# Kernel optimization log

Hardware: AMD Instinct MI355X
Metric: run time of the kernel (lower is better)

The kernel has to match this reference:

```python
import jax, jax.numpy as jnp
import numpy as np

N = 100000          # nodes
E = 3200000         # edges (avg degree 32)
C = 64              # classes
NUM_CORR = 10
ALPHA_CORR = 0.979
NUM_SMOOTH = 10
ALPHA_SMOOTH = 0.756


def setup_inputs() -> dict:
    key = jax.random.key(0)
    k1, k2, k3, k4, k5 = jax.random.split(key, 5)
    # soft predictions: rows sum to 1 (asserted in the torch code)
    y_soft = jax.nn.softmax(jax.random.normal(k1, (N, C), dtype=jnp.float32), axis=-1)
    labels = jax.random.randint(k2, (N,), 0, C)
    y_true = jax.nn.one_hot(labels, C, dtype=jnp.float32)
    src = jax.random.randint(k3, (E,), 0, N)
    dst = jax.random.randint(k4, (E,), 0, N)
    mask = jax.random.uniform(k5, (N,)) < 0.5
    return {"y_soft": y_soft, "y_true": y_true, "src": src, "dst": dst, "mask": mask}


def _propagate(y, src, dst, norm, num_layers, alpha, lo, hi):
    # DAD: y <- clip(last + alpha * D^-1/2 A D^-1/2 y, lo, hi) repeated
    last = (1.0 - alpha) * y
    for _ in range(num_layers):
        y = norm * y                                            # D^-1/2 y
        h = jax.ops.segment_sum(y[src], dst, num_segments=N)    # A (SpMM via copy_u/sum)
        y = alpha * h * norm                                    # alpha D^-1/2 (.)
        y = jnp.clip(last + y, lo, hi)                          # post_step clamp
    return y


def reference(y_soft, y_true, src, dst, mask):
    dt = y_soft.dtype
    degs = jnp.clip(jax.ops.segment_sum(jnp.ones((E,), dt), dst, num_segments=N), 1.0, None)
    norm = (degs ** -0.5)[:, None]                              # [N,1]
    m = mask[:, None]

    # ---- correct (autoscale=True) ----
    error = jnp.where(m, y_true - y_soft, jnp.zeros((), dt))    # zero off-mask
    smoothed_error = _propagate(error, src, dst, norm, NUM_CORR, ALPHA_CORR, -1.0, 1.0)
    numel = jnp.sum(mask).astype(dt)
    sigma = jnp.sum(jnp.abs(error)) / numel                     # error is 0 off-mask
    scale = sigma / jnp.sum(jnp.abs(smoothed_error), axis=1, keepdims=True)
    scale = jnp.where(jnp.isinf(scale) | (scale > 1000.0), jnp.ones((), dt), scale)
    result = y_soft + scale * smoothed_error
    result = jnp.where(jnp.isnan(result), y_soft, result)

    # ---- smooth ----
    y = jnp.where(m, y_true, result)                            # y_soft[mask] = y_true
    out = _propagate(y, src, dst, norm, NUM_SMOOTH, ALPHA_SMOOTH, 0.0, 1.0)
    return out
```

## Files before the change

kernel.cpp:

```cpp
#include <hip/hip_runtime.h>
#include <hip/hip_bf16.h>

#define NN 100000
#define EE 3200000
#define CC 64
#define NC (NN*CC)
#define SCAN_BLOCKS 391
#define ERR_BLOCKS 6250

__device__ __forceinline__ float ldf(const void* p, long i, int isbf) {
    if (isbf) {
        unsigned int u = ((const unsigned short*)p)[i];
        return __uint_as_float(u << 16);
    }
    return ((const float*)p)[i];
}

__device__ __forceinline__ float wave_sum(float a) {
    for (int m = 1; m < 64; m <<= 1) a += __shfl_xor(a, m, 64);
    return a;
}

__device__ __forceinline__ unsigned pack_bf16(float a, float b) {
    unsigned ua = __float_as_uint(a); ua = (ua + 0x7FFFu + ((ua >> 16) & 1u)) >> 16;
    unsigned ub = __float_as_uint(b); ub = (ub + 0x7FFFu + ((ub >> 16) & 1u)) >> 16;
    return ua | (ub << 16);
}

__global__ void detect_kernel(const void* ytrue, const void* mask, int* flags) {
    int t = threadIdx.x;
    const unsigned int* w = (const unsigned int*)ytrue;
    int nb = 0, nm = 0;
    for (int i = t; i < 16384; i += 256)
        if ((w[i] & 0xFFFFu) == 0x3F80u) nb = 1;
    const unsigned char* mb = (const unsigned char*)mask;
    for (int i = t; i < 4096; i += 256)
        if ((i & 3) != 0 && mb[i] != 0) nm = 1;
    if (nb) atomicOr(&flags[0], 1);
    if (nm) atomicOr(&flags[1], 1);
}

__global__ void prep_kernel(const void* ytrue, const void* mask, const int* flags,
                            int* __restrict__ label, float* __restrict__ mask01) {
    int gt = blockIdx.x * blockDim.x + threadIdx.x;
    int node = gt >> 6, lane = gt & 63;
    if (node >= NN) return;
    int isbf = flags[0];
    float tv = ldf(ytrue, (long)node * CC + lane, isbf);
    unsigned long long b = __ballot(tv > 0.5f);
    if (lane == 0) {
        label[node] = (b == 0ull) ? 0 : (__ffsll((long long)b) - 1);
        int mv = flags[1] ? (int)((const unsigned char*)mask)[node] : ((const int*)mask)[node];
        mask01[node] = mv ? 1.f : 0.f;
    }
}

__global__ void deg_kernel(const int* __restrict__ dst, int* __restrict__ degi) {
    int e = blockIdx.x * blockDim.x + threadIdx.x;
    if (e < EE) atomicAdd(&degi[dst[e]], 1);
}

__global__ void norm_kernel(const int* __restrict__ degi, float* __restrict__ norm) {
    int n = blockIdx.x * blockDim.x + threadIdx.x;
    if (n < NN) {
        int d = degi[n]; if (d < 1) d = 1;
        norm[n] = rsqrtf((float)d);
    }
}

__global__ void scan1_kernel(const int* __restrict__ degi, int* __restrict__ partials) {
    int t = threadIdx.x, i = blockIdx.x * 256 + t;
    __shared__ int sm[256];
    sm[t] = (i < NN) ? degi[i] : 0; __syncthreads();
    for (int s = 128; s > 0; s >>= 1) {
        if (t < s) sm[t] += sm[t + s];
        __syncthreads();
    }
    if (t == 0) partials[blockIdx.x] = sm[0];
}

__global__ void scan2_kernel(const int* __restrict__ partials, int* __restrict__ chunk_off) {
    int t = threadIdx.x;
    __shared__ int sm[512];
    int v = (t < SCAN_BLOCKS) ? partials[t] : 0;
    sm[t] = v; __syncthreads();
    for (int off = 1; off < 512; off <<= 1) {
        int x = (t >= off) ? sm[t - off] : 0;
        __syncthreads();
        sm[t] += x;
        __syncthreads();
    }
    chunk_off[t] = sm[t] - v;
}

__global__ void scan3_kernel(const int* __restrict__ degi, const int* __restrict__ chunk_off,
                             int* __restrict__ row_ptr, int* __restrict__ cursor) {
    int t = threadIdx.x, b = blockIdx.x, i = b * 256 + t;
    __shared__ int sm[256];
    int v = (i < NN) ? degi[i] : 0;
    sm[t] = v; __syncthreads();
    for (int off = 1; off < 256; off <<= 1) {
        int x = (t >= off) ? sm[t - off] : 0;
        __syncthreads();
        sm[t] += x;
        __syncthreads();
    }
    int base = chunk_off[b];
    if (i < NN) {
        int ex = base + sm[t] - v;
        row_ptr[i] = ex; cursor[i] = ex;
    }
    if (i == NN - 1) row_ptr[NN] = base + sm[t];
}

__global__ void fill_kernel(const int* __restrict__ src, const int* __restrict__ dst,
                            int* __restrict__ cursor, int* __restrict__ csr_src) {
    int e = blockIdx.x * blockDim.x + threadIdx.x;
    if (e < EE) {
        int pos = atomicAdd(&cursor[dst[e]], 1);
        csr_src[pos] = src[e];
    }
}

__global__ void err_kernel(const void* ysoft, const int* flags, const int* __restrict__ label,
                           const float* __restrict__ mask01, const float* __restrict__ norm,
                           float* __restrict__ base, unsigned* __restrict__ curn,
                           float* __restrict__ err_part) {
    int i4 = blockIdx.x * 256 + threadIdx.x;
    int node = i4 >> 4;
    int isbf = flags[0];
    float m = mask01[node];
    int lab = label[node];
    float nrm = norm[node];
    int c0 = (i4 & 15) * 4;
    float4 e;
    if (isbf) {
        ushort4 u = ((const ushort4*)ysoft)[i4];
        e.x = __uint_as_float((unsigned)u.x << 16);
        e.y = __uint_as_float((unsigned)u.y << 16);
        e.z = __uint_as_float((unsigned)u.z << 16);
        e.w = __uint_as_float((unsigned)u.w << 16);
    } else {
        e = ((const float4*)ysoft)[i4];
    }
    e.x = (m != 0.f) ? ((c0 + 0 == lab) ? 1.f : 0.f) - e.x : 0.f;
    e.y = (m != 0.f) ? ((c0 + 1 == lab) ? 1.f : 0.f) - e.y : 0.f;
    e.z = (m != 0.f) ? ((c0 + 2 == lab) ? 1.f : 0.f) - e.z : 0.f;
    e.w = (m != 0.f) ? ((c0 + 3 == lab) ? 1.f : 0.f) - e.w : 0.f;
    ((float4*)base)[i4] = e;
    ((uint2*)curn)[i4] = make_uint2(pack_bf16(e.x * nrm, e.y * nrm),
                                    pack_bf16(e.z * nrm, e.w * nrm));
    float a = fabsf(e.x) + fabsf(e.y) + fabsf(e.z) + fabsf(e.w);
    a = wave_sum(a);
    __shared__ float sm[4];
    if ((threadIdx.x & 63) == 0) sm[threadIdx.x >> 6] = a;
    __syncthreads();
    if (threadIdx.x == 0) err_part[blockIdx.x] = sm[0] + sm[1] + sm[2] + sm[3];
}

__global__ void reduce_kernel(const float* __restrict__ mask01,
                              const float* __restrict__ err_part, float* __restrict__ scal) {
    int t = threadIdx.x;
    float s0 = 0.f, s1 = 0.f;
    for (int i = t; i < NN; i += 1024) s0 += mask01[i];
    for (int i = t; i < ERR_BLOCKS; i += 1024) s1 += err_part[i];
    __shared__ float a0[1024], a1[1024];
    a0[t] = s0; a1[t] = s1; __syncthreads();
    for (int s = 512; s > 0; s >>= 1) {
        if (t < s) { a0[t] += a0[t + s]; a1[t] += a1[t + s]; }
        __syncthreads();
    }
    if (t == 0) { scal[0] = a0[0]; scal[1] = a1[0]; }
}

__global__ void gather_kernel(const int* __restrict__ row_ptr, const int* __restrict__ csr_src,
                              const unsigned* __restrict__ curn, const float* __restrict__ base,
                              const float* __restrict__ norm, void* __restrict__ out,
                              float* __restrict__ rowsum, const int* flags,
                              float alpha, float lo, float hi, int mode) {
    int gt = blockIdx.x * blockDim.x + threadIdx.x;
    int node = gt >> 6, lane = gt & 63;
    if (node >= NN) return;
    int hl = lane & 31;
    int half = lane >> 5;
    int beg = row_ptr[node], end = row_ptr[node + 1];
    float acc0 = 0.f, acc1 = 0.f, acc2 = 0.f, acc3 = 0.f;
    for (int eb = beg; eb < end; eb += 64) {
        int ne = end - eb; if (ne > 64) ne = 64;
        int sv = (eb + lane < end) ? csr_src[eb + lane] : 0;
        int j = 0;
        for (; j + 7 < ne; j += 8) {
            int sA = __shfl(sv, j + 0 + half, 64);
            int sB = __shfl(sv, j + 2 + half, 64);
            int sC = __shfl(sv, j + 4 + half, 64);
            int sD = __shfl(sv, j + 6 + half, 64);
            unsigned wA = curn[(long)sA * 32 + hl];
            unsigned wB = curn[(long)sB * 32 + hl];
            unsigned wC = curn[(long)sC * 32 + hl];
            unsigned wD = curn[(long)sD * 32 + hl];
            acc0 += __uint_as_float(wA << 16) + __uint_as_float(wC << 16);
            acc1 += __uint_as_float(wA & 0xFFFF0000u) + __uint_as_float(wC & 0xFFFF0000u);
            acc2 += __uint_as_float(wB << 16) + __uint_as_float(wD << 16);
            acc3 += __uint_as_float(wB & 0xFFFF0000u) + __uint_as_float(wD & 0xFFFF0000u);
        }
        for (; j < ne; j += 2) {
            int jj = j + half;
            float wt = (jj < ne) ? 1.f : 0.f;
            int s = __shfl(sv, (jj < ne) ? jj : j, 64);
            unsigned w = curn[(long)s * 32 + hl];
            acc0 += wt * __uint_as_float(w << 16);
            acc1 += wt * __uint_as_float(w & 0xFFFF0000u);
        }
    }
    acc0 += acc2; acc1 += acc3;
    acc0 += __shfl_xor(acc0, 32, 64);
    acc1 += __shfl_xor(acc1, 32, 64);

    float nrm = norm[node];
    long i2 = (long)node * 32 + hl;
    float2 b2 = ((const float2*)base)[i2];
    float v0 = (1.f - alpha) * b2.x + alpha * nrm * acc0;
    float v1 = (1.f - alpha) * b2.y + alpha * nrm * acc1;
    v0 = v0 < lo ? lo : (v0 > hi ? hi : v0);
    v1 = v1 < lo ? lo : (v1 > hi ? hi : v1);

    if (mode == 1) {
        float contrib = (lane < 32) ? (fabsf(v0) + fabsf(v1)) : 0.f;
        float rs = wave_sum(contrib);
        if (lane == 0) rowsum[node] = rs;
        if (lane < 32) ((float2*)out)[i2] = make_float2(v0, v1);
    } else if (mode == 0) {
        if (lane < 32) ((unsigned*)out)[i2] = pack_bf16(v0 * nrm, v1 * nrm);
    } else {
        if (lane < 32) {
            if (flags[0]) ((unsigned*)out)[i2] = pack_bf16(v0, v1);
            else          ((float2*)out)[i2] = make_float2(v0, v1);
        }
    }
}

__global__ void scale_kernel(const float* __restrict__ rowsum, const float* __restrict__ scal,
                             float* __restrict__ scale) {
    int n = blockIdx.x * blockDim.x + threadIdx.x;
    if (n >= NN) return;
    float sigma = scal[1] / scal[0];
    float s = sigma / rowsum[n];
    if (isinf(s) || s > 1000.f) s = 1.f;
    scale[n] = s;
}

__global__ void y0_kernel(const void* ysoft, const int* flags, const int* __restrict__ label,
                          const float* __restrict__ mask01, const float* __restrict__ scale,
                          const float* __restrict__ norm, const float* __restrict__ smoothed,
                          float* __restrict__ base, unsigned* __restrict__ curn) {
    int i4 = blockIdx.x * 256 + threadIdx.x;
    int node = i4 >> 4;
    int isbf = flags[0];
    float m = mask01[node];
    int lab = label[node];
    float nrm = norm[node], sc = scale[node];
    int c0 = (i4 & 15) * 4;
    float4 ys;
    if (isbf) {
        ushort4 u = ((const ushort4*)ysoft)[i4];
        ys.x = __uint_as_float((unsigned)u.x << 16);
        ys.y = __uint_as_float((unsigned)u.y << 16);
        ys.z = __uint_as_float((unsigned)u.z << 16);
        ys.w = __uint_as_float((unsigned)u.w << 16);
    } else {
        ys = ((const float4*)ysoft)[i4];
    }
    float4 sm = ((const float4*)smoothed)[i4];
    float rx = ys.x + sc * sm.x; if (isnan(rx)) rx = ys.x;
    float ry = ys.y + sc * sm.y; if (isnan(ry)) ry = ys.y;
    float rz = ys.z + sc * sm.z; if (isnan(rz)) rz = ys.z;
    float rw = ys.w + sc * sm.w; if (isnan(rw)) rw = ys.w;
    float4 y;
    y.x = (m != 0.f) ? ((c0 + 0 == lab) ? 1.f : 0.f) : rx;
    y.y = (m != 0.f) ? ((c0 + 1 == lab) ? 1.f : 0.f) : ry;
    y.z = (m != 0.f) ? ((c0 + 2 == lab) ? 1.f : 0.f) : rz;
    y.w = (m != 0.f) ? ((c0 + 3 == lab) ? 1.f : 0.f) : rw;
    ((float4*)base)[i4] = y;
    ((uint2*)curn)[i4] = make_uint2(pack_bf16(y.x * nrm, y.y * nrm),
                                    pack_bf16(y.z * nrm, y.w * nrm));
}

extern "C" void kernel_launch(void* const* d_in, const int* in_sizes, int n_in,
                              void* d_out, int out_size, void* d_ws, size_t ws_size,
                              hipStream_t stream) {
    const void* ysoft = d_in[0];
    const void* ytrue = d_in[1];
    const int* src = (const int*)d_in[2];
    const int* dst = (const int*)d_in[3];
    const void* mask = d_in[4];

    char* ws = (char*)d_ws;
    int*   flags     = (int*)ws;
    float* scal      = (float*)(ws + 64);
    int*   partials  = (int*)(ws + 4096);
    int*   chunk_off = (int*)(ws + 8192);
    float* err_part  = (float*)(ws + 12288);
    int*   degi      = (int*)(ws + 40960);
    size_t ZERO_BYTES = 40960 + (size_t)NN * 4;

    size_t off = (ZERO_BYTES + 255) & ~(size_t)255;
    int*   label   = (int*)(ws + off);   off += (size_t)NN * 4;
    float* mask01  = (float*)(ws + off); off += (size_t)NN * 4;
    float* norm    = (float*)(ws + off); off += (size_t)NN * 4;
    float* scale   = (float*)(ws + off); off += (size_t)NN * 4;
    float* rowsum  = (float*)(ws + off); off += (size_t)NN * 4;
    int*   row_ptr = (int*)(ws + off);   off += (size_t)(NN + 1) * 4;
    int*   cursor  = (int*)(ws + off);   off += (size_t)NN * 4;
    off = (off + 255) & ~(size_t)255;
    int*   csr_src  = (int*)(ws + off);      off += (size_t)EE * 4;
    off = (off + 255) & ~(size_t)255;
    float*    base     = (float*)(ws + off);    off += (size_t)NC * 4;
    float*    smoothed = (float*)(ws + off);    off += (size_t)NC * 4;
    unsigned* bufA     = (unsigned*)(ws + off); off += (size_t)NC * 2;
    unsigned* bufB     = (unsigned*)(ws + off); off += (size_t)NC * 2;

    hipMemsetAsync(ws, 0, ZERO_BYTES, stream);

    detect_kernel<<<1, 256, 0, stream>>>(ytrue, mask, flags);
    prep_kernel<<<(NN * 64 + 255) / 256, 256, 0, stream>>>(ytrue, mask, flags, label, mask01);
    deg_kernel<<<(EE + 255) / 256, 256, 0, stream>>>(dst, degi);
    norm_kernel<<<(NN + 255) / 256, 256, 0, stream>>>(degi, norm);
    scan1_kernel<<<SCAN_BLOCKS, 256, 0, stream>>>(degi, partials);
    scan2_kernel<<<1, 512, 0, stream>>>(partials, chunk_off);
    scan3_kernel<<<SCAN_BLOCKS, 256, 0, stream>>>(degi, chunk_off, row_ptr, cursor);
    fill_kernel<<<(EE + 255) / 256, 256, 0, stream>>>(src, dst, cursor, csr_src);
    err_kernel<<<ERR_BLOCKS, 256, 0, stream>>>(ysoft, flags, label, mask01, norm, base, bufA, err_part);
    reduce_kernel<<<1, 1024, 0, stream>>>(mask01, err_part, scal);

    const int gather_blocks = (NN * 64 + 255) / 256;

    unsigned* cur = bufA; unsigned* nxt = bufB;
    for (int l = 0; l < 10; l++) {
        int mode = (l < 9) ? 0 : 1;
        void* o = (l < 9) ? (void*)nxt : (void*)smoothed;
        gather_kernel<<<gather_blocks, 256, 0, stream>>>(row_ptr, csr_src, cur, base, norm, o,
                                                         rowsum, flags, 0.979f, -1.f, 1.f, mode);
        unsigned* t = cur; cur = nxt; nxt = t;
    }

    scale_kernel<<<(NN + 255) / 256, 256, 0, stream>>>(rowsum, scal, scale);
    y0_kernel<<<ERR_BLOCKS, 256, 0, stream>>>(ysoft, flags, label, mask01, scale, norm,
                                              smoothed, base, bufA);

    cur = bufA; nxt = bufB;
    for (int l = 0; l < 10; l++) {
        int mode = (l < 9) ? 0 : 3;
        void* o = (l < 9) ? (void*)nxt : (void*)d_out;
        gather_kernel<<<gather_blocks, 256, 0, stream>>>(row_ptr, csr_src, cur, base, norm, o,
                                                         rowsum, flags, 0.756f, 0.f, 1.f, mode);
        unsigned* t = cur; cur = nxt; nxt = t;
    }
}
```

Baseline: 1.790 ms.

## Split feature columns into four chunk-major slabs and gather per chunk

Re-lays out the propagated feature buffers as four 16-column chunks stored chunk-major. Each gather block then processes one chunk for four nodes, with 8 lanes per neighbor and 8 neighbors per step. The aim is a smaller per-iteration working set, about 3.2 MB of bf16 per chunk, so the random neighbor gathers hit cache better. In exchange each edge list is read four times, row sums are accumulated with atomics into a zeroed buffer, and the final output is scattered back to row-major order. Non-temporal loads are used for the edge indices and the base values.

Result: slower. 3.920 ms (+119.0%).

```diff
diff --git a/kernel.cpp b/kernel.cpp
--- a/kernel.cpp
+++ b/kernel.cpp
@@ -7,6 +7,7 @@
 #define NC (NN*CC)
 #define SCAN_BLOCKS 391
 #define ERR_BLOCKS 6250
+
 
 __device__ __forceinline__ float ldf(const void* p, long i, int isbf) {
     if (isbf) {
@@ -128,11 +129,14 @@
                            float* __restrict__ err_part) {
     int i4 = blockIdx.x * 256 + threadIdx.x;
     int node = i4 >> 4;
+    int w16 = i4 & 15;
+    int chunk = w16 >> 2, q = w16 & 3;
+    long ci = ((long)chunk * NN + node) * 4 + q;
     int isbf = flags[0];
     float m = mask01[node];
     int lab = label[node];
     float nrm = norm[node];
-    int c0 = (i4 & 15) * 4;
+    int c0 = w16 * 4;
     float4 e;
     if (isbf) {
         ushort4 u = ((const ushort4*)ysoft)[i4];
@@ -147,8 +151,8 @@
     e.y = (m != 0.f) ? ((c0 + 1 == lab) ? 1.f : 0.f) - e.y : 0.f;
     e.z = (m != 0.f) ? ((c0 + 2 == lab) ? 1.f : 0.f) - e.z : 0.f;
     e.w = (m != 0.f) ? ((c0 + 3 == lab) ? 1.f : 0.f) - e.w : 0.f;
-    ((float4*)base)[i4] = e;
-    ((uint2*)curn)[i4] = make_uint2(pack_bf16(e.x * nrm, e.y * nrm),
+    ((float4*)base)[ci] = e;
+    ((uint2*)curn)[ci] = make_uint2(pack_bf16(e.x * nrm, e.y * nrm),
                                     pack_bf16(e.z * nrm, e.w * nrm));
     float a = fabsf(e.x) + fabsf(e.y) + fabsf(e.z) + fabsf(e.w);
     a = wave_sum(a);
@@ -173,68 +177,76 @@
     if (t == 0) { scal[0] = a0[0]; scal[1] = a1[0]; }
 }
 
-__global__ void gather_kernel(const int* __restrict__ row_ptr, const int* __restrict__ csr_src,
-                              const unsigned* __restrict__ curn, const float* __restrict__ base,
-                              const float* __restrict__ norm, void* __restrict__ out,
-                              float* __restrict__ rowsum, const int* flags,
-                              float alpha, float lo, float hi, int mode) {
-    int gt = blockIdx.x * blockDim.x + threadIdx.x;
-    int node = gt >> 6, lane = gt & 63;
-    if (node >= NN) return;
-    int hl = lane & 31;
-    int half = lane >> 5;
+__global__ void __launch_bounds__(256)
+gather_kernel(const int* __restrict__ row_ptr, const int* __restrict__ csr_src,
+              const unsigned* __restrict__ curn, const float* __restrict__ base,
+              const float* __restrict__ norm, void* __restrict__ out,
+              float* __restrict__ rowsum, const int* flags,
+              float alpha, float lo, float hi, int mode) {
+    int chunk = blockIdx.x & 3;
+    int node = (blockIdx.x >> 2) * 4 + (threadIdx.x >> 6);
+    int lane = threadIdx.x & 63;
+    int group = lane >> 3, gl = lane & 7;
+    long cbase = (long)chunk * NN;
+    const unsigned* __restrict__ cw = curn + cbase * 8;
     int beg = row_ptr[node], end = row_ptr[node + 1];
-    float acc0 = 0.f, acc1 = 0.f, acc2 = 0.f, acc3 = 0.f;
+    float acc0 = 0.f, acc1 = 0.f;
     for (int eb = beg; eb < end; eb += 64) {
         int ne = end - eb; if (ne > 64) ne = 64;
-        int sv = (eb + lane < end) ? csr_src[eb + lane] : 0;
+        int sv = (eb + lane < end) ? __builtin_nontemporal_load(csr_src + eb + lane) : 0;
         int j = 0;
-        for (; j + 7 < ne; j += 8) {
-            int sA = __shfl(sv, j + 0 + half, 64);
-            int sB = __shfl(sv, j + 2 + half, 64);
-            int sC = __shfl(sv, j + 4 + half, 64);
-            int sD = __shfl(sv, j + 6 + half, 64);
-            unsigned wA = curn[(long)sA * 32 + hl];
-            unsigned wB = curn[(long)sB * 32 + hl];
-            unsigned wC = curn[(long)sC * 32 + hl];
-            unsigned wD = curn[(long)sD * 32 + hl];
-            acc0 += __uint_as_float(wA << 16) + __uint_as_float(wC << 16);
-            acc1 += __uint_as_float(wA & 0xFFFF0000u) + __uint_as_float(wC & 0xFFFF0000u);
-            acc2 += __uint_as_float(wB << 16) + __uint_as_float(wD << 16);
-            acc3 += __uint_as_float(wB & 0xFFFF0000u) + __uint_as_float(wD & 0xFFFF0000u);
+        for (; j + 31 < ne; j += 32) {
+            int s0 = __shfl(sv, j + group, 64);
+            int s1 = __shfl(sv, j + 8 + group, 64);
+            int s2 = __shfl(sv, j + 16 + group, 64);
+            int s3 = __shfl(sv, j + 24 + group, 64);
+            unsigned w0 = cw[(long)s0 * 8 + gl];
+            unsigned w1 = cw[(long)s1 * 8 + gl];
+            unsigned w2 = cw[(long)s2 * 8 + gl];
+            unsigned w3 = cw[(long)s3 * 8 + gl];
+            acc0 += __uint_as_float(w0 << 16) + __uint_as_float(w1 << 16)
+                  + __uint_as_float(w2 << 16) + __uint_as_float(w3 << 16);
+            acc1 += __uint_as_float(w0 & 0xFFFF0000u) + __uint_as_float(w1 & 0xFFFF0000u)
+                  + __uint_as_float(w2 & 0xFFFF0000u) + __uint_as_float(w3 & 0xFFFF0000u);
         }
-        for (; j < ne; j += 2) {
-            int jj = j + half;
-            float wt = (jj < ne) ? 1.f : 0.f;
-            int s = __shfl(sv, (jj < ne) ? jj : j, 64);
-            unsigned w = curn[(long)s * 32 + hl];
+        for (; j < ne; j += 8) {
+            int ej = j + group;
+            int s = __shfl(sv, (ej < ne) ? ej : j, 64);
+            float wt = (ej < ne) ? 1.f : 0.f;
+            unsigned w = cw[(long)s * 8 + gl];
             acc0 += wt * __uint_as_float(w << 16);
             acc1 += wt * __uint_as_float(w & 0xFFFF0000u);
         }
     }
-    acc0 += acc2; acc1 += acc3;
-    acc0 += __shfl_xor(acc0, 32, 64);
-    acc1 += __shfl_xor(acc1, 32, 64);
+    acc0 += __shfl_xor(acc0, 8, 64);  acc1 += __shfl_xor(acc1, 8, 64);
+    acc0 += __shfl_xor(acc0, 16, 64); acc1 += __shfl_xor(acc1, 16, 64);
+    acc0 += __shfl_xor(acc0, 32, 64); acc1 += __shfl_xor(acc1, 32, 64);
 
     float nrm = norm[node];
-    long i2 = (long)node * 32 + hl;
-    float2 b2 = ((const float2*)base)[i2];
+    long i2 = (cbase + node) * 8 + gl;
+    float2 b2;
+    {
+        const float* bp = base + i2 * 2;
+        b2.x = __builtin_nontemporal_load(bp);
+        b2.y = __builtin_nontemporal_load(bp + 1);
+    }
     float v0 = (1.f - alpha) * b2.x + alpha * nrm * acc0;
     float v1 = (1.f - alpha) * b2.y + alpha * nrm * acc1;
     v0 = v0 < lo ? lo : (v0 > hi ? hi : v0);
     v1 = v1 < lo ? lo : (v1 > hi ? hi : v1);
 
-    if (mode == 1) {
-        float contrib = (lane < 32) ? (fabsf(v0) + fabsf(v1)) : 0.f;
-        float rs = wave_sum(contrib);
-        if (lane == 0) rowsum[node] = rs;
-        if (lane < 32) ((float2*)out)[i2] = make_float2(v0, v1);
-    } else if (mode == 0) {
-        if (lane < 32) ((unsigned*)out)[i2] = pack_bf16(v0 * nrm, v1 * nrm);
+    if (mode == 0) {
+        if (lane < 8) ((unsigned*)out)[i2] = pack_bf16(v0 * nrm, v1 * nrm);
+    } else if (mode == 1) {
+        float rs = fabsf(v0) + fabsf(v1);
+        rs += __shfl_xor(rs, 1, 64); rs += __shfl_xor(rs, 2, 64); rs += __shfl_xor(rs, 4, 64);
+        if (lane == 0) atomicAdd(&rowsum[node], rs);
+        if (lane < 8) ((float2*)out)[i2] = make_float2(v0, v1);
     } else {
-        if (lane < 32) {
-            if (flags[0]) ((unsigned*)out)[i2] = pack_bf16(v0, v1);
-            else          ((float2*)out)[i2] = make_float2(v0, v1);
+        if (lane < 8) {
+            long oi = (long)node * 32 + chunk * 8 + gl;
+            if (flags[0]) ((unsigned*)out)[oi] = pack_bf16(v0, v1);
+            else          ((float2*)out)[oi] = make_float2(v0, v1);
         }
     }
 }
@@ -255,11 +267,14 @@
                           float* __restrict__ base, unsigned* __restrict__ curn) {
     int i4 = blockIdx.x * 256 + threadIdx.x;
     int node = i4 >> 4;
+    int w16 = i4 & 15;
+    int chunk = w16 >> 2, q = w16 & 3;
+    long ci = ((long)chunk * NN + node) * 4 + q;
     int isbf = flags[0];
     float m = mask01[node];
     int lab = label[node];
     float nrm = norm[node], sc = scale[node];
-    int c0 = (i4 & 15) * 4;
+    int c0 = w16 * 4;
     float4 ys;
     if (isbf) {
         ushort4 u = ((const ushort4*)ysoft)[i4];
@@ -270,7 +285,7 @@
     } else {
         ys = ((const float4*)ysoft)[i4];
     }
-    float4 sm = ((const float4*)smoothed)[i4];
+    float4 sm = ((const float4*)smoothed)[ci];
     float rx = ys.x + sc * sm.x; if (isnan(rx)) rx = ys.x;
     float ry = ys.y + sc * sm.y; if (isnan(ry)) ry = ys.y;
     float rz = ys.z + sc * sm.z; if (isnan(rz)) rz = ys.z;
@@ -280,8 +295,8 @@
     y.y = (m != 0.f) ? ((c0 + 1 == lab) ? 1.f : 0.f) : ry;
     y.z = (m != 0.f) ? ((c0 + 2 == lab) ? 1.f : 0.f) : rz;
     y.w = (m != 0.f) ? ((c0 + 3 == lab) ? 1.f : 0.f) : rw;
-    ((float4*)base)[i4] = y;
-    ((uint2*)curn)[i4] = make_uint2(pack_bf16(y.x * nrm, y.y * nrm),
+    ((float4*)base)[ci] = y;
+    ((uint2*)curn)[ci] = make_uint2(pack_bf16(y.x * nrm, y.y * nrm),
                                     pack_bf16(y.z * nrm, y.w * nrm));
 }
 
@@ -301,14 +316,14 @@
     int*   chunk_off = (int*)(ws + 8192);
     float* err_part  = (float*)(ws + 12288);
     int*   degi      = (int*)(ws + 40960);
-    size_t ZERO_BYTES = 40960 + (size_t)NN * 4;
+    float* rowsum    = (float*)(ws + 40960 + (size_t)NN * 4);
+    size_t ZERO_BYTES = 40960 + (size_t)NN * 8;
 
     size_t off = (ZERO_BYTES + 255) & ~(size_t)255;
     int*   label   = (int*)(ws + off);   off += (size_t)NN * 4;
     float* mask01  = (float*)(ws + off); off += (size_t)NN * 4;
     float* norm    = (float*)(ws + off); off += (size_t)NN * 4;
     float* scale   = (float*)(ws + off); off += (size_t)NN * 4;
-    float* rowsum  = (float*)(ws + off); off += (size_t)NN * 4;
     int*   row_ptr = (int*)(ws + off);   off += (size_t)(NN + 1) * 4;
     int*   cursor  = (int*)(ws + off);   off += (size_t)NN * 4;
     off = (off + 255) & ~(size_t)255;
@@ -332,7 +347,7 @@
     err_kernel<<<ERR_BLOCKS, 256, 0, stream>>>(ysoft, flags, label, mask01, norm, base, bufA, err_part);
     reduce_kernel<<<1, 1024, 0, stream>>>(mask01, err_part, scal);
 
-    const int gather_blocks = (NN * 64 + 255) / 256;
+    const int gather_blocks = NN;
 
     unsigned* cur = bufA; unsigned* nxt = bufB;
     for (int l = 0; l < 10; l++) {
```

## Build CSR via two-level bucket sort instead of global atomic counting sort

Applied to the files above, without the earlier changes.

Replaces the global-atomic degree count, three-kernel scan and atomic scatter fill with a bucketed two-pass sort. Edges are first binned by dst>>8 using shared-memory histograms and staging into a temporary buffer that aliases `base`. Each bucket is then sorted locally in LDS to produce row_ptr, norm and csr_src. The aim is to cut contended global atomics and scattered writes during CSR construction. It also folds scale_kernel into y0_kernel. The cost is extra passes over the edge list, 64KB of LDS staging per block, and a dependence on `base` not being needed before err_kernel.

After: 1.498 ms. 1.2x faster.

```diff
diff --git a/kernel.cpp b/kernel.cpp
--- a/kernel.cpp
+++ b/kernel.cpp
@@ -5,8 +5,10 @@
 #define EE 3200000
 #define CC 64
 #define NC (NN*CC)
-#define SCAN_BLOCKS 391
 #define ERR_BLOCKS 6250
+#define NB 391
+#define TILE 8192
+#define NTILE 391
 
 __device__ __forceinline__ float ldf(const void* p, long i, int isbf) {
     if (isbf) {
@@ -55,34 +57,25 @@
     }
 }
 
-__global__ void deg_kernel(const int* __restrict__ dst, int* __restrict__ degi) {
-    int e = blockIdx.x * blockDim.x + threadIdx.x;
-    if (e < EE) atomicAdd(&degi[dst[e]], 1);
-}
-
-__global__ void norm_kernel(const int* __restrict__ degi, float* __restrict__ norm) {
-    int n = blockIdx.x * blockDim.x + threadIdx.x;
-    if (n < NN) {
-        int d = degi[n]; if (d < 1) d = 1;
-        norm[n] = rsqrtf((float)d);
-    }
-}
-
-__global__ void scan1_kernel(const int* __restrict__ degi, int* __restrict__ partials) {
-    int t = threadIdx.x, i = blockIdx.x * 256 + t;
-    __shared__ int sm[256];
-    sm[t] = (i < NN) ? degi[i] : 0; __syncthreads();
-    for (int s = 128; s > 0; s >>= 1) {
-        if (t < s) sm[t] += sm[t + s];
-        __syncthreads();
-    }
-    if (t == 0) partials[blockIdx.x] = sm[0];
-}
-
-__global__ void scan2_kernel(const int* __restrict__ partials, int* __restrict__ chunk_off) {
+__global__ void histA_kernel(const int* __restrict__ dst, int* __restrict__ bucket_tot) {
+    __shared__ int hist[NB];
+    int t = threadIdx.x;
+    for (int b = t; b < NB; b += 256) hist[b] = 0;
+    __syncthreads();
+    int e0 = blockIdx.x * TILE;
+    int n = EE - e0; if (n > TILE) n = TILE;
+    for (int k = t; k < n; k += 256)
+        atomicAdd(&hist[dst[e0 + k] >> 8], 1);
+    __syncthreads();
+    for (int b = t; b < NB; b += 256)
+        if (hist[b]) atomicAdd(&bucket_tot[b], hist[b]);
+}
+
+__global__ void bscan_kernel(const int* __restrict__ bucket_tot,
+                             int* __restrict__ bucket_base, int* __restrict__ bucket_fill) {
     int t = threadIdx.x;
     __shared__ int sm[512];
-    int v = (t < SCAN_BLOCKS) ? partials[t] : 0;
+    int v = (t < NB) ? bucket_tot[t] : 0;
     sm[t] = v; __syncthreads();
     for (int off = 1; off < 512; off <<= 1) {
         int x = (t >= off) ? sm[t - off] : 0;
@@ -90,14 +83,66 @@
         sm[t] += x;
         __syncthreads();
     }
-    chunk_off[t] = sm[t] - v;
-}
-
-__global__ void scan3_kernel(const int* __restrict__ degi, const int* __restrict__ chunk_off,
-                             int* __restrict__ row_ptr, int* __restrict__ cursor) {
-    int t = threadIdx.x, b = blockIdx.x, i = b * 256 + t;
-    __shared__ int sm[256];
-    int v = (i < NN) ? degi[i] : 0;
+    int ex = sm[t] - v;
+    if (t <= NB) { bucket_base[t] = ex; bucket_fill[t] = ex; }
+}
+
+__global__ void __launch_bounds__(512)
+binA_kernel(const int* __restrict__ src, const int* __restrict__ dst,
+            int* __restrict__ bucket_fill, uint2* __restrict__ tmp) {
+    __shared__ uint2 stage[TILE];
+    __shared__ int hist[512], hofs[512], curL[512], gbase[512];
+    __shared__ int sm[512];
+    int t = threadIdx.x;
+    int e0 = blockIdx.x * TILE;
+    int n = EE - e0; if (n > TILE) n = TILE;
+
+    hist[t] = 0;
+    __syncthreads();
+    for (int k = t; k < n; k += 512)
+        atomicAdd(&hist[dst[e0 + k] >> 8], 1);
+    __syncthreads();
+    int v = hist[t];
+    sm[t] = v; __syncthreads();
+    for (int off = 1; off < 512; off <<= 1) {
+        int x = (t >= off) ? sm[t - off] : 0;
+        __syncthreads();
+        sm[t] += x;
+        __syncthreads();
+    }
+    hofs[t] = sm[t] - v;
+    curL[t] = sm[t] - v;
+    __syncthreads();
+    for (int k = t; k < n; k += 512) {
+        int s = src[e0 + k], d = dst[e0 + k];
+        int b = d >> 8;
+        int p = atomicAdd(&curL[b], 1);
+        stage[p] = make_uint2((unsigned)s, (unsigned)d);
+    }
+    if (t < NB) {
+        int c = hist[t];
+        gbase[t] = c ? atomicAdd(&bucket_fill[t], c) : 0;
+    }
+    __syncthreads();
+    for (int k = t; k < n; k += 512) {
+        uint2 pr = stage[k];
+        int b = (int)(pr.y >> 8);
+        tmp[gbase[b] + (k - hofs[b])] = pr;
+    }
+}
+
+__global__ void __launch_bounds__(256)
+csrB_kernel(const uint2* __restrict__ tmp, const int* __restrict__ bucket_base,
+            int* __restrict__ row_ptr, float* __restrict__ norm, int* __restrict__ csr_src) {
+    __shared__ int deg[256], cur[256], sm[256];
+    int t = threadIdx.x, b = blockIdx.x;
+    int ebeg = bucket_base[b], eend = bucket_base[b + 1];
+    deg[t] = 0;
+    __syncthreads();
+    for (int i = ebeg + t; i < eend; i += 256)
+        atomicAdd(&deg[tmp[i].y & 255u], 1);
+    __syncthreads();
+    int v = deg[t];
     sm[t] = v; __syncthreads();
     for (int off = 1; off < 256; off <<= 1) {
         int x = (t >= off) ? sm[t - off] : 0;
@@ -105,20 +150,20 @@
         sm[t] += x;
         __syncthreads();
     }
-    int base = chunk_off[b];
-    if (i < NN) {
-        int ex = base + sm[t] - v;
-        row_ptr[i] = ex; cursor[i] = ex;
-    }
-    if (i == NN - 1) row_ptr[NN] = base + sm[t];
-}
-
-__global__ void fill_kernel(const int* __restrict__ src, const int* __restrict__ dst,
-                            int* __restrict__ cursor, int* __restrict__ csr_src) {
-    int e = blockIdx.x * blockDim.x + threadIdx.x;
-    if (e < EE) {
-        int pos = atomicAdd(&cursor[dst[e]], 1);
-        csr_src[pos] = src[e];
+    int lofs = sm[t] - v;
+    int node = b * 256 + t;
+    if (node < NN) {
+        row_ptr[node] = ebeg + lofs;
+        int d = v; if (d < 1) d = 1;
+        norm[node] = rsqrtf((float)d);
+    }
+    if (b == NB - 1 && t == 0) row_ptr[NN] = EE;
+    cur[t] = lofs;
+    __syncthreads();
+    for (int i = ebeg + t; i < eend; i += 256) {
+        uint2 pr = tmp[i];
+        int p = atomicAdd(&cur[pr.y & 255u], 1);
+        csr_src[ebeg + p] = (int)pr.x;
     }
 }
 
@@ -239,18 +284,9 @@
     }
 }
 
-__global__ void scale_kernel(const float* __restrict__ rowsum, const float* __restrict__ scal,
-                             float* __restrict__ scale) {
-    int n = blockIdx.x * blockDim.x + threadIdx.x;
-    if (n >= NN) return;
-    float sigma = scal[1] / scal[0];
-    float s = sigma / rowsum[n];
-    if (isinf(s) || s > 1000.f) s = 1.f;
-    scale[n] = s;
-}
-
 __global__ void y0_kernel(const void* ysoft, const int* flags, const int* __restrict__ label,
-                          const float* __restrict__ mask01, const float* __restrict__ scale,
+                          const float* __restrict__ mask01, const float* __restrict__ rowsum,
+                          const float* __restrict__ scal,
                           const float* __restrict__ norm, const float* __restrict__ smoothed,
                           float* __restrict__ base, unsigned* __restrict__ curn) {
     int i4 = blockIdx.x * 256 + threadIdx.x;
@@ -258,7 +294,10 @@
     int isbf = flags[0];
     float m = mask01[node];
     int lab = label[node];
-    float nrm = norm[node], sc = scale[node];
+    float nrm = norm[node];
+    float sigma = scal[1] / scal[0];
+    float sc = sigma / rowsum[node];
+    if (isinf(sc) || sc > 1000.f) sc = 1.f;
     int c0 = (i4 & 15) * 4;
     float4 ys;
     if (isbf) {
@@ -295,40 +334,38 @@
     const void* mask = d_in[4];
 
     char* ws = (char*)d_ws;
-    int*   flags     = (int*)ws;
-    float* scal      = (float*)(ws + 64);
-    int*   partials  = (int*)(ws + 4096);
-    int*   chunk_off = (int*)(ws + 8192);
-    float* err_part  = (float*)(ws + 12288);
-    int*   degi      = (int*)(ws + 40960);
-    size_t ZERO_BYTES = 40960 + (size_t)NN * 4;
-
-    size_t off = (ZERO_BYTES + 255) & ~(size_t)255;
+    int*   flags       = (int*)ws;
+    float* scal        = (float*)(ws + 64);
+    int*   bucket_tot  = (int*)(ws + 4096);
+    size_t ZERO_BYTES  = 16384;
+    int*   bucket_base = (int*)(ws + 16384);
+    int*   bucket_fill = (int*)(ws + 20480);
+    float* err_part    = (float*)(ws + 24576);
+
+    size_t off = 24576 + (size_t)ERR_BLOCKS * 4;
+    off = (off + 255) & ~(size_t)255;
     int*   label   = (int*)(ws + off);   off += (size_t)NN * 4;
     float* mask01  = (float*)(ws + off); off += (size_t)NN * 4;
     float* norm    = (float*)(ws + off); off += (size_t)NN * 4;
-    float* scale   = (float*)(ws + off); off += (size_t)NN * 4;
     float* rowsum  = (float*)(ws + off); off += (size_t)NN * 4;
     int*   row_ptr = (int*)(ws + off);   off += (size_t)(NN + 1) * 4;
-    int*   cursor  = (int*)(ws + off);   off += (size_t)NN * 4;
     off = (off + 255) & ~(size_t)255;
-    int*   csr_src  = (int*)(ws + off);      off += (size_t)EE * 4;
+    int*   csr_src = (int*)(ws + off);   off += (size_t)EE * 4;
     off = (off + 255) & ~(size_t)255;
     float*    base     = (float*)(ws + off);    off += (size_t)NC * 4;
     float*    smoothed = (float*)(ws + off);    off += (size_t)NC * 4;
     unsigned* bufA     = (unsigned*)(ws + off); off += (size_t)NC * 2;
     unsigned* bufB     = (unsigned*)(ws + off); off += (size_t)NC * 2;
+    uint2* tmp = (uint2*)base;
 
     hipMemsetAsync(ws, 0, ZERO_BYTES, stream);
 
     detect_kernel<<<1, 256, 0, stream>>>(ytrue, mask, flags);
     prep_kernel<<<(NN * 64 + 255) / 256, 256, 0, stream>>>(ytrue, mask, flags, label, mask01);
-    deg_kernel<<<(EE + 255) / 256, 256, 0, stream>>>(dst, degi);
-    norm_kernel<<<(NN + 255) / 256, 256, 0, stream>>>(degi, norm);
-    scan1_kernel<<<SCAN_BLOCKS, 256, 0, stream>>>(degi, partials);
-    scan2_kernel<<<1, 512, 0, stream>>>(partials, chunk_off);
-    scan3_kernel<<<SCAN_BLOCKS, 256, 0, stream>>>(degi, chunk_off, row_ptr, cursor);
-    fill_kernel<<<(EE + 255) / 256, 256, 0, stream>>>(src, dst, cursor, csr_src);
+    histA_kernel<<<NTILE, 256, 0, stream>>>(dst, bucket_tot);
+    bscan_kernel<<<1, 512, 0, stream>>>(bucket_tot, bucket_base, bucket_fill);
+    binA_kernel<<<NTILE, 512, 0, stream>>>(src, dst, bucket_fill, tmp);
+    csrB_kernel<<<NB, 256, 0, stream>>>(tmp, bucket_base, row_ptr, norm, csr_src);
     err_kernel<<<ERR_BLOCKS, 256, 0, stream>>>(ysoft, flags, label, mask01, norm, base, bufA, err_part);
     reduce_kernel<<<1, 1024, 0, stream>>>(mask01, err_part, scal);
 
@@ -343,8 +380,7 @@
         unsigned* t = cur; cur = nxt; nxt = t;
     }
 
-    scale_kernel<<<(NN + 255) / 256, 256, 0, stream>>>(rowsum, scal, scale);
-    y0_kernel<<<ERR_BLOCKS, 256, 0, stream>>>(ysoft, flags, label, mask01, scale, norm,
+    y0_kernel<<<ERR_BLOCKS, 256, 0, stream>>>(ysoft, flags, label, mask01, rowsum, scal, norm,
                                               smoothed, base, bufA);
 
     cur = bufA; nxt = bufB;
```
